# Performance work log

Hardware: AMD Instinct MI355X
Metric: run time of the kernel (lower is better)

Reference implementation:

```python
import jax, jax.numpy as jnp
import numpy as np

IN_SIZE = 768
FC_SIZE = 3072
H = 12
ATT = IN_SIZE // H
EPS = 1e-5


def setup_inputs() -> dict:
    key = jax.random.key(0)
    ks = jax.random.split(key, 12)
    B, S = 4, 1024
    x = jax.random.normal(ks[0], (B, S, IN_SIZE), dtype=jnp.float32)
    mask = jax.random.randint(ks[1], (B, S, S), 0, 2, dtype=jnp.int32)
    s = 1.0 / np.sqrt(IN_SIZE)
    WQ = jax.random.normal(ks[2], (IN_SIZE, IN_SIZE), dtype=jnp.float32) * s
    WK = jax.random.normal(ks[3], (IN_SIZE, IN_SIZE), dtype=jnp.float32) * s
    WV = jax.random.normal(ks[4], (IN_SIZE, IN_SIZE), dtype=jnp.float32) * s
    Wfc = jax.random.normal(ks[5], (IN_SIZE, IN_SIZE), dtype=jnp.float32) * s
    W1 = jax.random.normal(ks[6], (IN_SIZE, FC_SIZE), dtype=jnp.float32) * s
    b1 = jnp.zeros((FC_SIZE,), dtype=jnp.float32)
    W2 = jax.random.normal(ks[7], (FC_SIZE, IN_SIZE), dtype=jnp.float32) / np.sqrt(FC_SIZE)
    b2 = jnp.zeros((IN_SIZE,), dtype=jnp.float32)
    g1 = jnp.ones((IN_SIZE,), dtype=jnp.float32)
    be1 = jnp.zeros((IN_SIZE,), dtype=jnp.float32)
    g2 = jnp.ones((IN_SIZE,), dtype=jnp.float32)
    be2 = jnp.zeros((IN_SIZE,), dtype=jnp.float32)
    return dict(x=x, mask=mask, WQ=WQ, WK=WK, WV=WV, Wfc=Wfc,
                W1=W1, b1=b1, W2=W2, b2=b2, g1=g1, be1=be1, g2=g2, be2=be2)


def _layernorm(x, g, b):
    mu = jnp.mean(x, axis=-1, keepdims=True)
    var = jnp.var(x, axis=-1, keepdims=True)
    return (x - mu) * jax.lax.rsqrt(var + EPS) * g + b


def reference(x, mask, WQ, WK, WV, Wfc, W1, b1, W2, b2, g1, be1, g2, be2):
    B, S, D = x.shape
    # NOTE: original code scales by sqrt(h), not sqrt(head_dim)
    scale = np.sqrt(H).astype(np.float32)
    Q = (x @ WQ).reshape(B, S, H, ATT).transpose(0, 2, 1, 3)  # [B,H,S,d]
    K = (x @ WK).reshape(B, S, H, ATT).transpose(0, 2, 1, 3)
    V = (x @ WV).reshape(B, S, H, ATT).transpose(0, 2, 1, 3)
    alpha = jnp.einsum('bhqd,bhkd->bhqk', Q, K) / scale
    alpha = jnp.where(mask[:, None, :, :] == 0, -1e9, alpha)
    alpha = jax.nn.softmax(alpha, axis=-1)
    att = jnp.einsum('bhqk,bhkd->bhqd', alpha, V)
    att = att.transpose(0, 2, 1, 3).reshape(B, S, D)
    att = att @ Wfc
    norm_att = _layernorm(att + x, g1, be1)
    lin = jax.nn.relu(norm_att @ W1 + b1) @ W2 + b2
    out = _layernorm(lin + norm_att, g2, be2)
    return out
```

## Files before the change

kernel.cpp:

```cpp
#include <hip/hip_runtime.h>
#include <stdint.h>

#define DMODEL 768
#define DFC    3072
#define NHEAD  12
#define DHEAD  64
#define BSZ    4
#define SEQ    1024
#define NTOK   (BSZ*SEQ)
#define QKVN   (3*DMODEL)

typedef unsigned short u16;
typedef unsigned int   u32;
typedef unsigned long long u64;
typedef __bf16 bf16_t;
typedef bf16_t bf16x8 __attribute__((ext_vector_type(8)));
typedef float  f32x4  __attribute__((ext_vector_type(4)));

__device__ __forceinline__ u16 f2b(float f) {
  u32 u = __builtin_bit_cast(u32, f);
  u = (u + 0x7FFFu + ((u >> 16) & 1u)) >> 16;
  return (u16)u;
}
__device__ __forceinline__ float b2f(u16 u) {
  return __builtin_bit_cast(float, (u32)u << 16);
}

__device__ __forceinline__ void gload_lds16(const void* g, void* l) {
  __builtin_amdgcn_global_load_lds(
      (const __attribute__((address_space(1))) void*)g,
      (__attribute__((address_space(3))) void*)l, 16, 0, 0);
}

__global__ __launch_bounds__(256) void mega_prep(
    const float* __restrict__ x, u16* __restrict__ XB,
    const float* __restrict__ WQ, const float* __restrict__ WK,
    const float* __restrict__ WV, const float* __restrict__ Wfc,
    const float* __restrict__ W1, const float* __restrict__ W2,
    u16* __restrict__ WQKVT, u16* __restrict__ WFCT,
    u16* __restrict__ W1T, u16* __restrict__ W2T,
    const int* __restrict__ mask, u64* __restrict__ MP) {
  __shared__ float tile[32][33];
  int bid = blockIdx.x, tid = threadIdx.x;

  if (bid < 3072) {
    int i = bid * 256 + tid;
    float4 v = ((const float4*)x)[i];
    ushort4 o;
    o.x = f2b(v.x); o.y = f2b(v.y); o.z = f2b(v.z); o.w = f2b(v.w);
    ((ushort4*)XB)[i] = o;
    return;
  }
  if (bid >= 9984) {
    int t = bid - 9984;
    int w = tid >> 6, lane = tid & 63;
    int idx = t * 4 + w;
    u64 bal = __ballot(mask[(size_t)idx * 64 + lane] != 0);
    if (lane == 0) MP[idx] = bal;
    return;
  }
  const float* in; u16* outp; int K, N, bx, by;
  if (bid < 5376) {
    int r = bid - 3072, which = r / 576, t = r % 576;
    in = which == 0 ? WQ : which == 1 ? WK : which == 2 ? WV : Wfc;
    outp = which < 3 ? WQKVT + (size_t)which * DMODEL * DMODEL : WFCT;
    K = DMODEL; N = DMODEL; bx = (t % 24) * 32; by = (t / 24) * 32;
  } else if (bid < 7680) {
    int t = bid - 5376;
    in = W1; outp = W1T; K = DMODEL; N = DFC;
    bx = (t % 96) * 32; by = (t / 96) * 32;
  } else {
    int t = bid - 7680;
    in = W2; outp = W2T; K = DFC; N = DMODEL;
    bx = (t % 24) * 32; by = (t / 24) * 32;
  }
  int tx = tid & 31, ty = tid >> 5;
#pragma unroll
  for (int i = 0; i < 4; ++i)
    tile[ty + i * 8][tx] = in[(size_t)(by + ty + i * 8) * N + bx + tx];
  __syncthreads();
#pragma unroll
  for (int i = 0; i < 4; ++i)
    outp[(size_t)(bx + ty + i * 8) * K + by + tx] = f2b(tile[tx][ty + i * 8]);
}

__global__ __launch_bounds__(256) void build_vt(const u16* __restrict__ QKVM,
                                                u16* __restrict__ VT) {
  __shared__ u16 t[64][72];
  int st = blockIdx.x, h = blockIdx.y, b = blockIdx.z;
  int tid = threadIdx.x;
  const u16* src = QKVM + ((size_t)(b * SEQ + st * 64)) * QKVN + 2 * DMODEL + h * DHEAD;
#pragma unroll
  for (int p = 0; p < 2; ++p) {
    int s = (p * 256 + tid) >> 3, c8 = tid & 7;
    *(uint4*)&t[s][c8 * 8] = *(const uint4*)&src[(size_t)s * QKVN + c8 * 8];
  }
  __syncthreads();
  u16* dst = VT + ((size_t)(b * NHEAD + h) * 64) * SEQ + st * 64;
#pragma unroll
  for (int p = 0; p < 2; ++p) {
    int d = (p * 256 + tid) >> 3, s8 = tid & 7;
    union { uint4 v; u16 s[8]; } o;
#pragma unroll
    for (int j = 0; j < 8; ++j) o.s[j] = t[s8 * 8 + j][d];
    *(uint4*)&dst[(size_t)d * SEQ + s8 * 8] = o.v;
  }
}

template <int MODE, int SPLIT>
__global__ __launch_bounds__(256) void gemm_bt(const u16* __restrict__ A,
                                               const u16* __restrict__ Bt,
                                               void* __restrict__ Cout,
                                               const float* __restrict__ bias,
                                               u16* __restrict__ pA, u16* __restrict__ pB,
                                               int M, int N, int K) {
  __shared__ __align__(16) u16 ldsA[2][128 * 32];
  __shared__ __align__(16) u16 ldsB[2][128 * 32];
  int tid = threadIdx.x;
  int lane = tid & 63, l15 = lane & 15, g = lane >> 4;
  int w = tid >> 6, wm = w >> 1, wn = w & 1;
  int m0 = blockIdx.y * 128, n0 = blockIdx.x * 128;
  int KS = K / SPLIT;
  int k0 = blockIdx.z * KS;
  int NT = KS >> 5;

  f32x4 acc[4][4];
#pragma unroll
  for (int i = 0; i < 4; ++i)
#pragma unroll
    for (int j = 0; j < 4; ++j) acc[i][j] = (f32x4){0.f, 0.f, 0.f, 0.f};

  const u16* gabase = A + (size_t)m0 * K + k0;
  const u16* gbbase = Bt + (size_t)n0 * K + k0;
  int wbase = tid & ~63;
  int lswz = (lane & 3) ^ ((lane >> 3) & 3);

  auto stage = [&](int kt, int buf) {
#pragma unroll
    for (int p = 0; p < 2; ++p) {
      int c = p * 256 + tid;
      int row = c >> 2;
      size_t goff = (size_t)row * K + kt * 32 + lswz * 8;
      gload_lds16(gabase + goff, &ldsA[buf][(p * 256 + wbase) * 8]);
      gload_lds16(gbbase + goff, &ldsB[buf][(p * 256 + wbase) * 8]);
    }
  };

  int rswz = (l15 >> 1) & 3;

  stage(0, 0);
  __syncthreads();
  for (int kt = 0; kt < NT; ++kt) {
    int cur = kt & 1;
    if (kt + 1 < NT) stage(kt + 1, cur ^ 1);
    bf16x8 af[4], bfr[4];
#pragma unroll
    for (int i = 0; i < 4; ++i) {
      af[i]  = *(const bf16x8*)&ldsA[cur][(wm * 64 + i * 16 + l15) * 32 + (g ^ rswz) * 8];
      bfr[i] = *(const bf16x8*)&ldsB[cur][(wn * 64 + i * 16 + l15) * 32 + (g ^ rswz) * 8];
    }
#pragma unroll
    for (int i = 0; i < 4; ++i)
#pragma unroll
      for (int j = 0; j < 4; ++j)
        acc[i][j] = __builtin_amdgcn_mfma_f32_16x16x32_bf16(af[i], bfr[j], acc[i][j], 0, 0, 0);
    __syncthreads();
  }

  u16* pdst = nullptr;
  if (MODE == 5)
    pdst = ((blockIdx.z & 2) ? pB : pA) + (size_t)(blockIdx.z & 1) * M * N;
#pragma unroll
  for (int i = 0; i < 4; ++i) {
#pragma unroll
    for (int j = 0; j < 4; ++j) {
#pragma unroll
      for (int r = 0; r < 4; ++r) {
        int row = m0 + wm * 64 + i * 16 + g * 4 + r;
        int col = n0 + wn * 64 + j * 16 + l15;
        float v = acc[i][j][r];
        if (MODE == 2) {
          v += bias[col];
          v = v > 0.f ? v : 0.f;
        }
        if (MODE == 0 || MODE == 2)
          ((u16*)Cout)[(size_t)row * N + col] = f2b(v);
        else if (MODE == 4)
          ((float*)Cout)[(size_t)blockIdx.z * M * N + (size_t)row * N + col] = v;
        else
          pdst[(size_t)row * N + col] = f2b(v);
      }
    }
  }
}

__global__ __launch_bounds__(256) void attn_kernel(const u16* __restrict__ QKVM,
                                                   const u16* __restrict__ VT,
                                                   const u64* __restrict__ MP,
                                                   u16* __restrict__ Om) {
  __shared__ __align__(16) u16 ldsK[2][64 * 64];
  __shared__ __align__(16) u16 ldsV[2][64 * 64];
  __shared__ __align__(16) u16 P_lds[4][16][72];

  int qt = blockIdx.x, h = blockIdx.y, b = blockIdx.z;
  int tid = threadIdx.x, w = tid >> 6, lane = tid & 63;
  int l15 = lane & 15, g = lane >> 4, l7 = lane & 7;
  int q0 = qt * 64 + w * 16;

  const u16* Qb = QKVM + (size_t)(b * SEQ) * QKVN + h * DHEAD;
  const u16* Kb = QKVM + (size_t)(b * SEQ) * QKVN + DMODEL + h * DHEAD;
  const u16* Vb = VT + (size_t)(b * NHEAD + h) * 64 * SEQ;

  bf16x8 qf[2];
  qf[0] = *(const bf16x8*)&Qb[(size_t)(q0 + l15) * QKVN + g * 8];
  qf[1] = *(const bf16x8*)&Qb[(size_t)(q0 + l15) * QKVN + 32 + g * 8];

  int r8 = lane >> 3, sl = lane & 7, slg = sl ^ r8;

  auto stage = [&](int kt, int buf) {
#pragma unroll
    for (int p = 0; p < 2; ++p) {
      int c = p * 4 + w;
      int row = c * 8 + r8;
      gload_lds16(Kb + (size_t)(kt * 64 + row) * QKVN + slg * 8, &ldsK[buf][c * 512]);
      gload_lds16(Vb + (size_t)row * SEQ + kt * 64 + slg * 8, &ldsV[buf][c * 512]);
    }
  };

  f32x4 acc[4];
  float ps[4];
#pragma unroll
  for (int d = 0; d < 4; ++d) acc[d] = (f32x4){0.f, 0.f, 0.f, 0.f};
#pragma unroll
  for (int r = 0; r < 4; ++r) ps[r] = 0.f;

  const float SC2 = 0.41650835f;

  stage(0, 0);
  __syncthreads();

  for (int kt = 0; kt < SEQ / 64; ++kt) {
    int cur = kt & 1;
    if (kt + 1 < SEQ / 64) stage(kt + 1, cur ^ 1);

    u64 mw[4];
#pragma unroll
    for (int r = 0; r < 4; ++r)
      mw[r] = MP[((size_t)(b * SEQ + q0 + g * 4 + r) << 4) | kt];

    f32x4 s[4];
#pragma unroll
    for (int fn = 0; fn < 4; ++fn) s[fn] = (f32x4){0.f, 0.f, 0.f, 0.f};
#pragma unroll
    for (int kf = 0; kf < 2; ++kf)
#pragma unroll
      for (int fn = 0; fn < 4; ++fn) {
        bf16x8 kfrag = *(const bf16x8*)((const char*)&ldsK[cur][0] +
                         (fn * 16 + l15) * 128 + (((kf * 4 + g) ^ l7) << 4));
        s[fn] = __builtin_amdgcn_mfma_f32_16x16x32_bf16(qf[kf], kfrag, s[fn], 0, 0, 0);
      }

#pragma unroll
    for (int fn = 0; fn < 4; ++fn) {
      u32 hv[4];
#pragma unroll
      for (int r = 0; r < 4; ++r)
        hv[r] = (fn & 2) ? (u32)(mw[r] >> 32) : (u32)mw[r];
      u32 bitpos = ((fn & 1) << 4) + l15;
#pragma unroll
      for (int r = 0; r < 4; ++r) {
        float pe = __builtin_amdgcn_exp2f(s[fn][r] * SC2);
        float p = ((hv[r] >> bitpos) & 1u) ? pe : 0.f;
        ps[r] += p;
        P_lds[w][g * 4 + r][fn * 16 + l15] = f2b(p);
      }
    }

#pragma unroll
    for (int kf2 = 0; kf2 < 2; ++kf2) {
      bf16x8 pf = *(const bf16x8*)((const char*)&P_lds[w][0][0] +
                    l15 * 144 + (kf2 * 32 + g * 8) * 2);
#pragma unroll
      for (int d = 0; d < 4; ++d) {
        bf16x8 vf = *(const bf16x8*)((const char*)&ldsV[cur][0] +
                      (d * 16 + l15) * 128 + (((kf2 * 4 + g) ^ l7) << 4));
        acc[d] = __builtin_amdgcn_mfma_f32_16x16x32_bf16(pf, vf, acc[d], 0, 0, 0);
      }
    }
    __syncthreads();
  }

#pragma unroll
  for (int r = 0; r < 4; ++r) {
#pragma unroll
    for (int off = 1; off < 16; off <<= 1) ps[r] += __shfl_xor(ps[r], off);
    ps[r] = 1.f / ps[r];
  }
#pragma unroll
  for (int d = 0; d < 4; ++d)
#pragma unroll
    for (int r = 0; r < 4; ++r) {
      float o = acc[d][r] * ps[r];
      Om[(size_t)(b * SEQ + q0 + g * 4 + r) * DMODEL + h * DHEAD + d * 16 + l15] = f2b(o);
    }
}

__global__ __launch_bounds__(256) void ln_sum2(const float* __restrict__ parts,
                                               const float* __restrict__ res,
                                               const float* __restrict__ gam,
                                               const float* __restrict__ bet,
                                               float* __restrict__ of,
                                               u16* __restrict__ ob) {
  int w = threadIdx.x >> 6, lane = threadIdx.x & 63;
  int row = blockIdx.x * 4 + w;
  const float* p0 = parts + (size_t)row * DMODEL;
  const float* p1 = parts + (size_t)NTOK * DMODEL + (size_t)row * DMODEL;
  const float* pr = res + (size_t)row * DMODEL;
  float4 v[3];
  float s = 0.f, s2 = 0.f;
#pragma unroll
  for (int j = 0; j < 3; ++j) {
    int c = lane * 4 + j * 256;
    float4 a = *(const float4*)&p0[c];
    float4 b = *(const float4*)&p1[c];
    float4 r = *(const float4*)&pr[c];
    float4 t = {a.x + b.x + r.x, a.y + b.y + r.y, a.z + b.z + r.z, a.w + b.w + r.w};
    v[j] = t;
    s += t.x + t.y + t.z + t.w;
    s2 += t.x * t.x + t.y * t.y + t.z * t.z + t.w * t.w;
  }
#pragma unroll
  for (int off = 32; off; off >>= 1) {
    s += __shfl_xor(s, off);
    s2 += __shfl_xor(s2, off);
  }
  float mu = s * (1.f / DMODEL);
  float var = s2 * (1.f / DMODEL) - mu * mu;
  float rs = rsqrtf(var + 1e-5f);
#pragma unroll
  for (int j = 0; j < 3; ++j) {
    int c = lane * 4 + j * 256;
    float4 gm = *(const float4*)&gam[c];
    float4 bt = *(const float4*)&bet[c];
    float4 o = {(v[j].x - mu) * rs * gm.x + bt.x, (v[j].y - mu) * rs * gm.y + bt.y,
                (v[j].z - mu) * rs * gm.z + bt.z, (v[j].w - mu) * rs * gm.w + bt.w};
    *(float4*)&of[(size_t)row * DMODEL + c] = o;
    ushort4 ub = {f2b(o.x), f2b(o.y), f2b(o.z), f2b(o.w)};
    *(ushort4*)&ob[(size_t)row * DMODEL + c] = ub;
  }
}

__global__ __launch_bounds__(256) void ln_sum4(const u16* __restrict__ pA,
                                               const u16* __restrict__ pB,
                                               const float* __restrict__ res,
                                               const float* __restrict__ badd,
                                               const float* __restrict__ gam,
                                               const float* __restrict__ bet,
                                               float* __restrict__ of) {
  int w = threadIdx.x >> 6, lane = threadIdx.x & 63;
  int row = blockIdx.x * 4 + w;
  size_t ro = (size_t)row * DMODEL;
  const size_t PS = (size_t)NTOK * DMODEL;
  float4 v[3];
  float s = 0.f, s2 = 0.f;
#pragma unroll
  for (int j = 0; j < 3; ++j) {
    int c = lane * 4 + j * 256;
    ushort4 u0 = *(const ushort4*)&pA[ro + c];
    ushort4 u1 = *(const ushort4*)&pA[PS + ro + c];
    ushort4 u2 = *(const ushort4*)&pB[ro + c];
    ushort4 u3 = *(const ushort4*)&pB[PS + ro + c];
    float4 r = *(const float4*)&res[ro + c];
    float4 bb = *(const float4*)&badd[c];
    float4 t = {b2f(u0.x) + b2f(u1.x) + b2f(u2.x) + b2f(u3.x) + r.x + bb.x,
                b2f(u0.y) + b2f(u1.y) + b2f(u2.y) + b2f(u3.y) + r.y + bb.y,
                b2f(u0.z) + b2f(u1.z) + b2f(u2.z) + b2f(u3.z) + r.z + bb.z,
                b2f(u0.w) + b2f(u1.w) + b2f(u2.w) + b2f(u3.w) + r.w + bb.w};
    v[j] = t;
    s += t.x + t.y + t.z + t.w;
    s2 += t.x * t.x + t.y * t.y + t.z * t.z + t.w * t.w;
  }
#pragma unroll
  for (int off = 32; off; off >>= 1) {
    s += __shfl_xor(s, off);
    s2 += __shfl_xor(s2, off);
  }
  float mu = s * (1.f / DMODEL);
  float var = s2 * (1.f / DMODEL) - mu * mu;
  float rs = rsqrtf(var + 1e-5f);
#pragma unroll
  for (int j = 0; j < 3; ++j) {
    int c = lane * 4 + j * 256;
    float4 gm = *(const float4*)&gam[c];
    float4 bt = *(const float4*)&bet[c];
    float4 o = {(v[j].x - mu) * rs * gm.x + bt.x, (v[j].y - mu) * rs * gm.y + bt.y,
                (v[j].z - mu) * rs * gm.z + bt.z, (v[j].w - mu) * rs * gm.w + bt.w};
    *(float4*)&of[ro + c] = o;
  }
}

extern "C" void kernel_launch(void* const* d_in, const int* in_sizes, int n_in,
                              void* d_out, int out_size, void* d_ws, size_t ws_size,
                              hipStream_t stream) {
  const float* x   = (const float*)d_in[0];
  const int*   msk = (const int*)d_in[1];
  const float* WQ  = (const float*)d_in[2];
  const float* WK  = (const float*)d_in[3];
  const float* WV  = (const float*)d_in[4];
  const float* Wfc = (const float*)d_in[5];
  const float* W1  = (const float*)d_in[6];
  const float* b1  = (const float*)d_in[7];
  const float* W2  = (const float*)d_in[8];
  const float* b2  = (const float*)d_in[9];
  const float* g1  = (const float*)d_in[10];
  const float* be1 = (const float*)d_in[11];
  const float* g2  = (const float*)d_in[12];
  const float* be2 = (const float*)d_in[13];
  float* out = (float*)d_out;

  char* ws = (char*)d_ws;
  u16*  XB    = (u16*)(ws + 0);
  u16*  WQKVT = (u16*)(ws + 6291456);
  u16*  WFCT  = (u16*)(ws + 9830400);
  u16*  W1T   = (u16*)(ws + 11010048);
  u16*  W2T   = (u16*)(ws + 15728640);
  u16*  QKVM  = (u16*)(ws + 20447232);
  u16*  VT    = (u16*)(ws + 39321600);
  u64*  MP    = (u64*)(ws + 45613056);
  float* NAF  = (float*)(ws + 46137344);
  u16*  NAB   = (u16*)(ws + 58720256);
  u16*   ATTO    = XB;
  float* PROJP   = (float*)QKVM;
  u16*   HMID    = QKVM;
  u16*   LINPA   = (u16*)(ws + 0);
  u16*   LINPB   = (u16*)(ws + 58720256);

  mega_prep<<<dim3(26368), dim3(256), 0, stream>>>(x, XB, WQ, WK, WV, Wfc, W1, W2,
                                                   WQKVT, WFCT, W1T, W2T, msk, MP);

  gemm_bt<0, 1><<<dim3(QKVN / 128, NTOK / 128, 1), dim3(256), 0, stream>>>(
      XB, WQKVT, QKVM, nullptr, nullptr, nullptr, NTOK, QKVN, DMODEL);
  build_vt<<<dim3(SEQ / 64, NHEAD, BSZ), dim3(256), 0, stream>>>(QKVM, VT);
  attn_kernel<<<dim3(SEQ / 64, NHEAD, BSZ), dim3(256), 0, stream>>>(QKVM, VT, MP, ATTO);

  gemm_bt<4, 2><<<dim3(DMODEL / 128, NTOK / 128, 2), dim3(256), 0, stream>>>(
      ATTO, WFCT, PROJP, nullptr, nullptr, nullptr, NTOK, DMODEL, DMODEL);
  ln_sum2<<<dim3(NTOK / 4), dim3(256), 0, stream>>>(PROJP, x, g1, be1, NAF, NAB);

  gemm_bt<2, 1><<<dim3(DFC / 128, NTOK / 128, 1), dim3(256), 0, stream>>>(
      NAB, W1T, HMID, b1, nullptr, nullptr, NTOK, DFC, DMODEL);
  gemm_bt<5, 4><<<dim3(DMODEL / 128, NTOK / 128, 4), dim3(256), 0, stream>>>(
      HMID, W2T, nullptr, nullptr, LINPA, LINPB, NTOK, DMODEL, DFC);
  ln_sum4<<<dim3(NTOK / 4), dim3(256), 0, stream>>>(LINPA, LINPB, NAF, b2, g2, be2, out);

  (void)in_sizes; (void)n_in; (void)out_size; (void)ws_size;
}
```

Before: 280.3 us.

## Remap workgroups for XCD locality and use transposed LDS reads for P in attention

Workgroup IDs in the GEMM and attention kernels are remapped round-robin across 8 groups, so blocks that share operands (same batch/head or neighbouring tiles) land on the same XCD and reuse its L2. The attention kernel's P tile is now stored column-major with packed bf16x2 writes and read back with ds_read_b64_tr_b16. V fragments are preloaded as bf16x4 halves, and float-to-bf16 conversion switches to the native __bf16 cast. The inline asm waitcnts and sched_barriers add serialization points, and the new fragment indexing must match the MFMA operand layout.

```diff
diff --git a/kernel.cpp b/kernel.cpp
--- a/kernel.cpp
+++ b/kernel.cpp
@@ -15,12 +15,13 @@
 typedef unsigned long long u64;
 typedef __bf16 bf16_t;
 typedef bf16_t bf16x8 __attribute__((ext_vector_type(8)));
+typedef bf16_t bf16x4 __attribute__((ext_vector_type(4)));
+typedef bf16_t bf16x2 __attribute__((ext_vector_type(2)));
 typedef float  f32x4  __attribute__((ext_vector_type(4)));
 
 __device__ __forceinline__ u16 f2b(float f) {
-  u32 u = __builtin_bit_cast(u32, f);
-  u = (u + 0x7FFFu + ((u >> 16) & 1u)) >> 16;
-  return (u16)u;
+  __bf16 h = (__bf16)f;
+  return __builtin_bit_cast(u16, h);
 }
 __device__ __forceinline__ float b2f(u16 u) {
   return __builtin_bit_cast(float, (u32)u << 16);
@@ -119,7 +120,13 @@
   int tid = threadIdx.x;
   int lane = tid & 63, l15 = lane & 15, g = lane >> 4;
   int w = tid >> 6, wm = w >> 1, wn = w & 1;
-  int m0 = blockIdx.y * 128, n0 = blockIdx.x * 128;
+
+  int gx = gridDim.x;
+  int bid = blockIdx.y * gx + blockIdx.x;
+  int nwg = gx * gridDim.y;
+  int wgid = ((nwg & 7) == 0) ? ((bid & 7) * (nwg >> 3) + (bid >> 3)) : bid;
+  int m0 = (wgid / gx) * 128, n0 = (wgid % gx) * 128;
+
   int KS = K / SPLIT;
   int k0 = blockIdx.z * KS;
   int NT = KS >> 5;
@@ -200,11 +207,15 @@
                                                    u16* __restrict__ Om) {
   __shared__ __align__(16) u16 ldsK[2][64 * 64];
   __shared__ __align__(16) u16 ldsV[2][64 * 64];
-  __shared__ __align__(16) u16 P_lds[4][16][72];
-
-  int qt = blockIdx.x, h = blockIdx.y, b = blockIdx.z;
+  __shared__ __align__(16) u16 Pt[4][64 * 16];
+
+  int bid = blockIdx.x;
+  int logical = (bid & 7) * 96 + (bid >> 3);
+  int qt = logical & 15, hb = logical >> 4;
+  int h = hb % NHEAD, b = hb / NHEAD;
+
   int tid = threadIdx.x, w = tid >> 6, lane = tid & 63;
-  int l15 = lane & 15, g = lane >> 4, l7 = lane & 7;
+  int l15 = lane & 15, g = lane >> 4;
   int q0 = qt * 64 + w * 16;
 
   const u16* Qb = QKVM + (size_t)(b * SEQ) * QKVN + h * DHEAD;
@@ -235,6 +246,9 @@
   for (int r = 0; r < 4; ++r) ps[r] = 0.f;
 
   const float SC2 = 0.41650835f;
+  u32 pbase = (u32)(uintptr_t)(__attribute__((address_space(3))) void*)&Pt[w][0]
+              + (u32)lane * 8u;
+  int l7s = l15 & 7;
 
   stage(0, 0);
   __syncthreads();
@@ -248,6 +262,17 @@
     for (int r = 0; r < 4; ++r)
       mw[r] = MP[((size_t)(b * SEQ + q0 + g * 4 + r) << 4) | kt];
 
+    bf16x4 vh[2][4][2];
+#pragma unroll
+    for (int kf2 = 0; kf2 < 2; ++kf2)
+#pragma unroll
+      for (int d = 0; d < 4; ++d)
+#pragma unroll
+        for (int hf = 0; hf < 2; ++hf) {
+          int slot = (kf2 * 4 + hf * 2 + (g >> 1)) ^ l7s;
+          vh[kf2][d][hf] = *(const bf16x4*)&ldsV[cur][(d * 16 + l15) * 64 + slot * 8 + (g & 1) * 4];
+        }
+
     f32x4 s[4];
 #pragma unroll
     for (int fn = 0; fn < 4; ++fn) s[fn] = (f32x4){0.f, 0.f, 0.f, 0.f};
@@ -256,35 +281,49 @@
 #pragma unroll
       for (int fn = 0; fn < 4; ++fn) {
         bf16x8 kfrag = *(const bf16x8*)((const char*)&ldsK[cur][0] +
-                         (fn * 16 + l15) * 128 + (((kf * 4 + g) ^ l7) << 4));
+                         (fn * 16 + l15) * 128 + (((kf * 4 + g) ^ l7s) << 4));
         s[fn] = __builtin_amdgcn_mfma_f32_16x16x32_bf16(qf[kf], kfrag, s[fn], 0, 0, 0);
       }
 
 #pragma unroll
     for (int fn = 0; fn < 4; ++fn) {
-      u32 hv[4];
-#pragma unroll
-      for (int r = 0; r < 4; ++r)
-        hv[r] = (fn & 2) ? (u32)(mw[r] >> 32) : (u32)mw[r];
       u32 bitpos = ((fn & 1) << 4) + l15;
+      float p[4];
 #pragma unroll
       for (int r = 0; r < 4; ++r) {
+        u32 hv = (fn & 2) ? (u32)(mw[r] >> 32) : (u32)mw[r];
         float pe = __builtin_amdgcn_exp2f(s[fn][r] * SC2);
-        float p = ((hv[r] >> bitpos) & 1u) ? pe : 0.f;
-        ps[r] += p;
-        P_lds[w][g * 4 + r][fn * 16 + l15] = f2b(p);
+        p[r] = ((hv >> bitpos) & 1u) ? pe : 0.f;
+        ps[r] += p[r];
       }
-    }
+      bf16x2 h0 = {(__bf16)p[0], (__bf16)p[1]};
+      bf16x2 h1 = {(__bf16)p[2], (__bf16)p[3]};
+      *(uint2*)&Pt[w][(fn * 16 + l15) * 16 + g * 4] =
+          make_uint2(__builtin_bit_cast(u32, h0), __builtin_bit_cast(u32, h1));
+    }
+
+    asm volatile("s_waitcnt lgkmcnt(0)" ::: "memory");
+    __builtin_amdgcn_sched_barrier(0);
+    uint2 t0, t1, t2, t3;
+    asm volatile("ds_read_b64_tr_b16 %0, %1 offset:0"    : "=v"(t0) : "v"(pbase) : "memory");
+    asm volatile("ds_read_b64_tr_b16 %0, %1 offset:512"  : "=v"(t1) : "v"(pbase) : "memory");
+    asm volatile("ds_read_b64_tr_b16 %0, %1 offset:1024" : "=v"(t2) : "v"(pbase) : "memory");
+    asm volatile("ds_read_b64_tr_b16 %0, %1 offset:1536" : "=v"(t3) : "v"(pbase) : "memory");
+    asm volatile("s_waitcnt lgkmcnt(0)" ::: "memory");
+    __builtin_amdgcn_sched_barrier(0);
+
+    union { uint2 u2[2]; bf16x8 v; } pa0, pa1;
+    pa0.u2[0] = t0; pa0.u2[1] = t1;
+    pa1.u2[0] = t2; pa1.u2[1] = t3;
 
 #pragma unroll
     for (int kf2 = 0; kf2 < 2; ++kf2) {
-      bf16x8 pf = *(const bf16x8*)((const char*)&P_lds[w][0][0] +
-                    l15 * 144 + (kf2 * 32 + g * 8) * 2);
+      bf16x8 pa = kf2 ? pa1.v : pa0.v;
 #pragma unroll
       for (int d = 0; d < 4; ++d) {
-        bf16x8 vf = *(const bf16x8*)((const char*)&ldsV[cur][0] +
-                      (d * 16 + l15) * 128 + (((kf2 * 4 + g) ^ l7) << 4));
-        acc[d] = __builtin_amdgcn_mfma_f32_16x16x32_bf16(pf, vf, acc[d], 0, 0, 0);
+        union { bf16x4 h[2]; bf16x8 v; } vf;
+        vf.h[0] = vh[kf2][d][0]; vf.h[1] = vh[kf2][d][1];
+        acc[d] = __builtin_amdgcn_mfma_f32_16x16x32_bf16(pa, vf.v, acc[d], 0, 0, 0);
       }
     }
     __syncthreads();
@@ -441,7 +480,7 @@
   gemm_bt<0, 1><<<dim3(QKVN / 128, NTOK / 128, 1), dim3(256), 0, stream>>>(
       XB, WQKVT, QKVM, nullptr, nullptr, nullptr, NTOK, QKVN, DMODEL);
   build_vt<<<dim3(SEQ / 64, NHEAD, BSZ), dim3(256), 0, stream>>>(QKVM, VT);
-  attn_kernel<<<dim3(SEQ / 64, NHEAD, BSZ), dim3(256), 0, stream>>>(QKVM, VT, MP, ATTO);
+  attn_kernel<<<dim3(BSZ * NHEAD * (SEQ / 64)), dim3(256), 0, stream>>>(QKVM, VT, MP, ATTO);
 
   gemm_bt<4, 2><<<dim3(DMODEL / 128, NTOK / 128, 2), dim3(256), 0, stream>>>(
       ATTO, WFCT, PROJP, nullptr, nullptr, nullptr, NTOK, DMODEL, DMODEL);
```

Result: faster. 274.1 us (-2.2%).
